# Kernel optimization log

Measured on AMD Instinct MI355X. Metric: run time of the kernel, lower is better.

## Reference

```python
import jax, jax.numpy as jnp
import numpy as np

TOP_K = 2
NUM_EXPERTS = 64
LOAD_BALANCE_ALPHA = 0.01
Z_LOSS_ALPHA = 1e-4
TEMPERATURE = 1.0  # buffer init, clamped to [0.1, 2.0] -> 1.0 (seq_len < 8192 branch)


def setup_inputs() -> dict:
    key = jax.random.key(0)
    k1, k2 = jax.random.split(key)
    x = jax.random.normal(k1, (4, 4096, 1024), dtype=jnp.float32)
    gate_w = jax.random.normal(k2, (NUM_EXPERTS, 1024), dtype=jnp.float32) * (1.0 / np.sqrt(1024))
    return {"x": x, "gate_w": gate_w}


def reference(x, gate_w):
    B, S, H = x.shape
    x_flat = x.reshape(-1, H)                      # [T, H], T = B*S
    logits = jnp.einsum('th,eh->te', x_flat, gate_w)  # [T, E]
    logits = logits / TEMPERATURE
    scores = jax.nn.softmax(logits, axis=-1)       # [T, E]
    # eval path: dynamic_top_k == top_k, no noise / capacity limitation
    top_scores, top_idx = jax.lax.top_k(scores, TOP_K)   # [T, K]
    top_scores = jax.nn.softmax(top_scores.astype(jnp.float32), axis=-1).astype(x.dtype)
    # load-balance loss: squared deviation of mean expert load from uniform
    expert_load = scores.mean(axis=0)              # [E]
    ideal = 1.0 / NUM_EXPERTS
    lb_loss = LOAD_BALANCE_ALPHA * NUM_EXPERTS * jnp.sum((expert_load - ideal) ** 2)
    # z-loss: mean squared logsumexp of gate logits
    z = jax.nn.logsumexp(logits, axis=-1)          # [T]
    z_loss = Z_LOSS_ALPHA * jnp.mean(z ** 2)
    total_loss = lb_loss + z_loss
    return top_scores, top_idx, total_loss
```

## Files before the change

kernel.cpp:

```cpp
#include <hip/hip_runtime.h>
#include <math.h>

#define T_TOK 16384
#define NEXP  64


__global__ void moe_prep(const float* __restrict__ gw, float* __restrict__ ws) {
    __shared__ float tile[64][65];
    const int b = blockIdx.x;
    const int tid = threadIdx.x;
    if (b == 0 && tid < 128) ws[tid] = 0.f;
#pragma unroll
    for (int it = 0; it < 16; ++it) {
        int idx = it * 256 + tid;
        int e = idx >> 6, kk = idx & 63;
        tile[e][kk] = gw[e * 1024 + b * 64 + kk];
    }
    __syncthreads();
#pragma unroll
    for (int it = 0; it < 16; ++it) {
        int idx = it * 256 + tid;
        int kk = idx >> 6, e = idx & 63;
        ws[128 + (b * 64 + kk) * 64 + e] = tile[e][kk];
    }
}

__launch_bounds__(1024, 4)
__global__ void moe_main(const float* __restrict__ x,
                         const float* __restrict__ wt,
                         float* __restrict__ acc_ws,
                         float* __restrict__ out) {
    __shared__ float xbuf[4096];
    __shared__ float wbuf[4096];
    __shared__ float sc[64 * 68];
    __shared__ float row_inv[64];
    __shared__ float colpart[16][64];
    __shared__ int   is_last;

    const int tid  = threadIdx.x;
    const int lane = tid & 63;
    const int wv   = tid >> 6;
    const int kq   = __builtin_amdgcn_readfirstlane(wv & 3);
    const int tile = __builtin_amdgcn_readfirstlane(wv >> 2);
    const int tt = tile >> 1, te = tile & 1;
    const int ta = lane >> 3;
    const int eb = lane & 7;
    const int tok0 = blockIdx.x << 6;

    const int rr = tid >> 4;
    const int cg = tid & 15;
    const float* gx = x + (((size_t)(tok0 + rr)) << 10) + ((cg >> 2) << 8) + ((cg & 3) << 2);
    const int xlo = (rr << 6) + ((cg ^ (rr & 15)) << 2);
    const float* gw = wt + ((((rr >> 4) << 8) + (rr & 15)) << 6) + (cg << 2);
    const int wlo = (rr << 6) + (cg << 2);

    float acc[16];
#pragma unroll
    for (int e = 0; e < 16; ++e) acc[e] = 0.f;

    const int t0 = (tt << 5) + (ta << 2);
    const float* xrow0 = xbuf + ((t0 + 0) << 6);
    const float* xrow1 = xbuf + ((t0 + 1) << 6);
    const float* xrow2 = xbuf + ((t0 + 2) << 6);
    const float* xrow3 = xbuf + ((t0 + 3) << 6);
    const int c0 = (t0 + 0) & 15, c1 = (t0 + 1) & 15;
    const int c2 = (t0 + 2) & 15, c3 = (t0 + 3) & 15;
    const int ebase = (te << 5) + (eb << 2);
    const float* wp = wbuf + (kq << 10) + ebase;
    const int cwb = kq << 2;

    float4 px = *(const float4*)gx;
    float4 pw = *(const float4*)gw;

#pragma unroll 1
    for (int s = 0; s < 16; ++s) {
        __syncthreads();
        *(float4*)(xbuf + xlo) = px;
        *(float4*)(wbuf + wlo) = pw;
        __syncthreads();
        if (s < 15) {
            px = *(const float4*)(gx + ((s + 1) << 4));
            pw = *(const float4*)(gw + ((s + 1) << 10));
        }
#pragma unroll
        for (int g4 = 0; g4 < 4; ++g4) {
            const int cw = cwb + g4;
            float4 xf0 = *(const float4*)(xrow0 + ((cw ^ c0) << 2));
            float4 xf1 = *(const float4*)(xrow1 + ((cw ^ c1) << 2));
            float4 xf2 = *(const float4*)(xrow2 + ((cw ^ c2) << 2));
            float4 xf3 = *(const float4*)(xrow3 + ((cw ^ c3) << 2));
            const float* wq = wp + (g4 << 8);
            float4 wf0 = *(const float4*)(wq);
            float4 wf1 = *(const float4*)(wq + 64);
            float4 wf2 = *(const float4*)(wq + 128);
            float4 wf3 = *(const float4*)(wq + 192);
            float xa[16] = {xf0.x, xf0.y, xf0.z, xf0.w,
                            xf1.x, xf1.y, xf1.z, xf1.w,
                            xf2.x, xf2.y, xf2.z, xf2.w,
                            xf3.x, xf3.y, xf3.z, xf3.w};
            float wa[16] = {wf0.x, wf0.y, wf0.z, wf0.w,
                            wf1.x, wf1.y, wf1.z, wf1.w,
                            wf2.x, wf2.y, wf2.z, wf2.w,
                            wf3.x, wf3.y, wf3.z, wf3.w};
#pragma unroll
            for (int i = 0; i < 4; ++i)
#pragma unroll
                for (int u = 0; u < 4; ++u) {
                    float xv = xa[(i << 2) + u];
#pragma unroll
                    for (int j = 0; j < 4; ++j)
                        acc[(i << 2) + j] = fmaf(xv, wa[(u << 2) + j], acc[(i << 2) + j]);
                }
        }
    }

    if (kq == 0) {
#pragma unroll
        for (int i = 0; i < 4; ++i) {
            float4 v = make_float4(acc[(i << 2)], acc[(i << 2) + 1],
                                   acc[(i << 2) + 2], acc[(i << 2) + 3]);
            *(float4*)(sc + (t0 + i) * 68 + ebase) = v;
        }
    }
    __syncthreads();
    if (kq == 1) {
#pragma unroll
        for (int i = 0; i < 4; ++i) {
            float4 o = *(float4*)(sc + (t0 + i) * 68 + ebase);
            o.x += acc[(i << 2)];     o.y += acc[(i << 2) + 1];
            o.z += acc[(i << 2) + 2]; o.w += acc[(i << 2) + 3];
            *(float4*)(sc + (t0 + i) * 68 + ebase) = o;
        }
    }
    __syncthreads();
    if (kq == 2) {
#pragma unroll
        for (int i = 0; i < 4; ++i) {
            float4 o = *(float4*)(sc + (t0 + i) * 68 + ebase);
            o.x += acc[(i << 2)];     o.y += acc[(i << 2) + 1];
            o.z += acc[(i << 2) + 2]; o.w += acc[(i << 2) + 3];
            *(float4*)(sc + (t0 + i) * 68 + ebase) = o;
        }
    }
    __syncthreads();
    if (kq == 3) {
#pragma unroll
        for (int i = 0; i < 4; ++i) {
            float4 o = *(float4*)(sc + (t0 + i) * 68 + ebase);
            o.x += acc[(i << 2)];     o.y += acc[(i << 2) + 1];
            o.z += acc[(i << 2) + 2]; o.w += acc[(i << 2) + 3];
            *(float4*)(sc + (t0 + i) * 68 + ebase) = o;
        }
    }
    __syncthreads();

    if (tid < 64) {
        const int r = tid;
        const float* srow = sc + r * 68;
        float v1 = -1e30f, v2 = -1e30f;
        int i1 = 0, i2 = 0;
        for (int j = 0; j < 64; ++j) {
            float l = srow[j];
            if (l > v1)      { v2 = v1; i2 = i1; v1 = l; i1 = j; }
            else if (l > v2) { v2 = l; i2 = j; }
        }
        float m = v1;
        float ssum = 0.f;
        for (int j = 0; j < 64; ++j) {
            float ev = expf(srow[j] - m);
            ssum += ev;
            sc[r * 68 + j] = ev;
        }
        float inv = 1.f / ssum;
        row_inv[r] = inv;
        float z = m + logf(ssum);
        float zsq = z * z;
#pragma unroll
        for (int off = 32; off > 0; off >>= 1) zsq += __shfl_down(zsq, off);
        if (lane == 0) atomicAdd(acc_ws + 64, zsq);

        float p1s = inv;
        float p2s = expf(v2 - m) * inv;
        float bb  = expf(p2s - p1s);
        float s1 = 1.f / (1.f + bb);
        float s2 = bb * s1;
        int t = tok0 + r;
        out[2 * t]     = s1;
        out[2 * t + 1] = s2;
        out[2 * T_TOK + 2 * t]     = (float)i1;
        out[2 * T_TOK + 2 * t + 1] = (float)i2;
    }
    __syncthreads();

    {
        int e  = tid & 63;
        int rg = tid >> 6;
        float sum = 0.f;
#pragma unroll
        for (int r2 = 0; r2 < 4; ++r2) {
            int row = (rg << 2) + r2;
            sum += sc[row * 68 + e] * row_inv[row];
        }
        colpart[rg][e] = sum;
    }
    __syncthreads();
    if (tid < 64) {
        float tot = 0.f;
#pragma unroll
        for (int rg = 0; rg < 16; ++rg) tot += colpart[rg][tid];
        atomicAdd(acc_ws + tid, tot);
    }

    __syncthreads();
    if (tid == 0) {
        __threadfence();
        int old = __hip_atomic_fetch_add((int*)(acc_ws + 66), 1,
                                         __ATOMIC_ACQ_REL, __HIP_MEMORY_SCOPE_AGENT);
        is_last = (old == 255) ? 1 : 0;
    }
    __syncthreads();
    if (is_last && tid < 64) {
        __threadfence();
        float load = __hip_atomic_load(acc_ws + tid, __ATOMIC_RELAXED,
                                       __HIP_MEMORY_SCOPE_AGENT) * (1.f / 16384.f);
        float d = load - (1.f / 64.f);
        float v = d * d;
#pragma unroll
        for (int off = 32; off > 0; off >>= 1) v += __shfl_down(v, off);
        if (tid == 0) {
            float zsum = __hip_atomic_load(acc_ws + 64, __ATOMIC_RELAXED,
                                           __HIP_MEMORY_SCOPE_AGENT);
            float lb = 0.01f * 64.f * v;
            float zl = 1e-4f * zsum * (1.f / 16384.f);
            out[4 * T_TOK] = lb + zl;
        }
    }
}

extern "C" void kernel_launch(void* const* d_in, const int* in_sizes, int n_in,
                              void* d_out, int out_size, void* d_ws, size_t ws_size,
                              hipStream_t stream) {
    const float* x  = (const float*)d_in[0];
    const float* gw = (const float*)d_in[1];
    float* out = (float*)d_out;
    float* ws  = (float*)d_ws;

    moe_prep<<<16, 256, 0, stream>>>(gw, ws);
    moe_main<<<256, 1024, 0, stream>>>(x, ws + 128, ws, out);
}
```

Baseline: 133.1 us.

## Split K across all 16 waves with 8x8 register tiles and three-buffer reduction

Each wave now owns a 4-wide K slice of every 64-wide K chunk and computes a full 64x64 token-by-expert tile, with each thread holding an 8x8 accumulator block instead of 4x4. The goal is more FMAs per shared-memory load and simpler LDS addressing: padded rows of 68 floats replace the XOR swizzle, and global loads become contiguous. The cost is that 16 partial tiles must now be summed. This is done in staged rounds into three LDS buffers (sc, xbuf, wbuf) and then merged. The extra barriers, more than 64 accumulator registers under the 1024-thread launch bound, and possible LDS bank conflicts from the strided x reads may offset the gain.

```diff
diff --git a/kernel.cpp b/kernel.cpp
--- a/kernel.cpp
+++ b/kernel.cpp
@@ -25,13 +25,36 @@
     }
 }
 
+__device__ __forceinline__ void pstore(float* B, const float (&a)[8][8],
+                                       int tg, int eg) {
+#pragma unroll
+    for (int i = 0; i < 8; ++i) {
+        float* p = B + (tg + 8 * i) * 68 + (eg << 3);
+        *(float4*)(p)     = make_float4(a[i][0], a[i][1], a[i][2], a[i][3]);
+        *(float4*)(p + 4) = make_float4(a[i][4], a[i][5], a[i][6], a[i][7]);
+    }
+}
+__device__ __forceinline__ void padd(float* B, const float (&a)[8][8],
+                                     int tg, int eg) {
+#pragma unroll
+    for (int i = 0; i < 8; ++i) {
+        float* p = B + (tg + 8 * i) * 68 + (eg << 3);
+        float4 v0 = *(float4*)(p);
+        float4 v1 = *(float4*)(p + 4);
+        v0.x += a[i][0]; v0.y += a[i][1]; v0.z += a[i][2]; v0.w += a[i][3];
+        v1.x += a[i][4]; v1.y += a[i][5]; v1.z += a[i][6]; v1.w += a[i][7];
+        *(float4*)(p)     = v0;
+        *(float4*)(p + 4) = v1;
+    }
+}
+
 __launch_bounds__(1024, 4)
 __global__ void moe_main(const float* __restrict__ x,
                          const float* __restrict__ wt,
                          float* __restrict__ acc_ws,
                          float* __restrict__ out) {
-    __shared__ float xbuf[4096];
-    __shared__ float wbuf[4096];
+    __shared__ float xbuf[64 * 68];
+    __shared__ float wbuf[64 * 68];
     __shared__ float sc[64 * 68];
     __shared__ float row_inv[64];
     __shared__ float colpart[16][64];
@@ -39,35 +62,25 @@
 
     const int tid  = threadIdx.x;
     const int lane = tid & 63;
-    const int wv   = tid >> 6;
-    const int kq   = __builtin_amdgcn_readfirstlane(wv & 3);
-    const int tile = __builtin_amdgcn_readfirstlane(wv >> 2);
-    const int tt = tile >> 1, te = tile & 1;
-    const int ta = lane >> 3;
-    const int eb = lane & 7;
+    const int wv   = __builtin_amdgcn_readfirstlane(tid >> 6);
+    const int tg   = lane & 7;
+    const int eg   = lane >> 3;
     const int tok0 = blockIdx.x << 6;
 
     const int rr = tid >> 4;
     const int cg = tid & 15;
-    const float* gx = x + (((size_t)(tok0 + rr)) << 10) + ((cg >> 2) << 8) + ((cg & 3) << 2);
-    const int xlo = (rr << 6) + ((cg ^ (rr & 15)) << 2);
-    const float* gw = wt + ((((rr >> 4) << 8) + (rr & 15)) << 6) + (cg << 2);
-    const int wlo = (rr << 6) + (cg << 2);
-
-    float acc[16];
-#pragma unroll
-    for (int e = 0; e < 16; ++e) acc[e] = 0.f;
-
-    const int t0 = (tt << 5) + (ta << 2);
-    const float* xrow0 = xbuf + ((t0 + 0) << 6);
-    const float* xrow1 = xbuf + ((t0 + 1) << 6);
-    const float* xrow2 = xbuf + ((t0 + 2) << 6);
-    const float* xrow3 = xbuf + ((t0 + 3) << 6);
-    const int c0 = (t0 + 0) & 15, c1 = (t0 + 1) & 15;
-    const int c2 = (t0 + 2) & 15, c3 = (t0 + 3) & 15;
-    const int ebase = (te << 5) + (eb << 2);
-    const float* wp = wbuf + (kq << 10) + ebase;
-    const int cwb = kq << 2;
+    const float* gx = x + (((size_t)(tok0 + rr)) << 10) + (cg << 2);
+    const float* gw = wt + (rr << 6) + (cg << 2);
+    const int lof = rr * 68 + (cg << 2);
+
+    float acc[8][8];
+#pragma unroll
+    for (int i = 0; i < 8; ++i)
+#pragma unroll
+        for (int j = 0; j < 8; ++j) acc[i][j] = 0.f;
+
+    const float* xr = xbuf + tg * 68 + (wv << 2);
+    const float* wr = wbuf + (wv * 4) * 68 + (eg << 3);
 
     float4 px = *(const float4*)gx;
     float4 pw = *(const float4*)gw;
@@ -75,82 +88,67 @@
 #pragma unroll 1
     for (int s = 0; s < 16; ++s) {
         __syncthreads();
-        *(float4*)(xbuf + xlo) = px;
-        *(float4*)(wbuf + wlo) = pw;
+        *(float4*)(xbuf + lof) = px;
+        *(float4*)(wbuf + lof) = pw;
         __syncthreads();
         if (s < 15) {
-            px = *(const float4*)(gx + ((s + 1) << 4));
-            pw = *(const float4*)(gw + ((s + 1) << 10));
-        }
-#pragma unroll
-        for (int g4 = 0; g4 < 4; ++g4) {
-            const int cw = cwb + g4;
-            float4 xf0 = *(const float4*)(xrow0 + ((cw ^ c0) << 2));
-            float4 xf1 = *(const float4*)(xrow1 + ((cw ^ c1) << 2));
-            float4 xf2 = *(const float4*)(xrow2 + ((cw ^ c2) << 2));
-            float4 xf3 = *(const float4*)(xrow3 + ((cw ^ c3) << 2));
-            const float* wq = wp + (g4 << 8);
-            float4 wf0 = *(const float4*)(wq);
-            float4 wf1 = *(const float4*)(wq + 64);
-            float4 wf2 = *(const float4*)(wq + 128);
-            float4 wf3 = *(const float4*)(wq + 192);
-            float xa[16] = {xf0.x, xf0.y, xf0.z, xf0.w,
-                            xf1.x, xf1.y, xf1.z, xf1.w,
-                            xf2.x, xf2.y, xf2.z, xf2.w,
-                            xf3.x, xf3.y, xf3.z, xf3.w};
-            float wa[16] = {wf0.x, wf0.y, wf0.z, wf0.w,
-                            wf1.x, wf1.y, wf1.z, wf1.w,
-                            wf2.x, wf2.y, wf2.z, wf2.w,
-                            wf3.x, wf3.y, wf3.z, wf3.w};
-#pragma unroll
-            for (int i = 0; i < 4; ++i)
-#pragma unroll
-                for (int u = 0; u < 4; ++u) {
-                    float xv = xa[(i << 2) + u];
-#pragma unroll
-                    for (int j = 0; j < 4; ++j)
-                        acc[(i << 2) + j] = fmaf(xv, wa[(u << 2) + j], acc[(i << 2) + j]);
-                }
-        }
-    }
-
-    if (kq == 0) {
-#pragma unroll
-        for (int i = 0; i < 4; ++i) {
-            float4 v = make_float4(acc[(i << 2)], acc[(i << 2) + 1],
-                                   acc[(i << 2) + 2], acc[(i << 2) + 3]);
-            *(float4*)(sc + (t0 + i) * 68 + ebase) = v;
-        }
-    }
-    __syncthreads();
-    if (kq == 1) {
-#pragma unroll
-        for (int i = 0; i < 4; ++i) {
-            float4 o = *(float4*)(sc + (t0 + i) * 68 + ebase);
-            o.x += acc[(i << 2)];     o.y += acc[(i << 2) + 1];
-            o.z += acc[(i << 2) + 2]; o.w += acc[(i << 2) + 3];
-            *(float4*)(sc + (t0 + i) * 68 + ebase) = o;
-        }
-    }
-    __syncthreads();
-    if (kq == 2) {
-#pragma unroll
-        for (int i = 0; i < 4; ++i) {
-            float4 o = *(float4*)(sc + (t0 + i) * 68 + ebase);
-            o.x += acc[(i << 2)];     o.y += acc[(i << 2) + 1];
-            o.z += acc[(i << 2) + 2]; o.w += acc[(i << 2) + 3];
-            *(float4*)(sc + (t0 + i) * 68 + ebase) = o;
-        }
-    }
-    __syncthreads();
-    if (kq == 3) {
-#pragma unroll
-        for (int i = 0; i < 4; ++i) {
-            float4 o = *(float4*)(sc + (t0 + i) * 68 + ebase);
-            o.x += acc[(i << 2)];     o.y += acc[(i << 2) + 1];
-            o.z += acc[(i << 2) + 2]; o.w += acc[(i << 2) + 3];
-            *(float4*)(sc + (t0 + i) * 68 + ebase) = o;
-        }
+            px = *(const float4*)(gx + ((s + 1) << 6));
+            pw = *(const float4*)(gw + ((s + 1) << 12));
+        }
+        float wa[4][8];
+#pragma unroll
+        for (int u = 0; u < 4; ++u) {
+            float4 q0 = *(const float4*)(wr + u * 68);
+            float4 q1 = *(const float4*)(wr + u * 68 + 4);
+            wa[u][0] = q0.x; wa[u][1] = q0.y; wa[u][2] = q0.z; wa[u][3] = q0.w;
+            wa[u][4] = q1.x; wa[u][5] = q1.y; wa[u][6] = q1.z; wa[u][7] = q1.w;
+        }
+#pragma unroll
+        for (int i = 0; i < 8; ++i) {
+            float4 xc = *(const float4*)(xr + i * 544);
+            float xa[4] = {xc.x, xc.y, xc.z, xc.w};
+#pragma unroll
+            for (int u = 0; u < 4; ++u) {
+                float xv = xa[u];
+#pragma unroll
+                for (int j = 0; j < 8; ++j)
+                    acc[i][j] = fmaf(xv, wa[u][j], acc[i][j]);
+            }
+        }
+    }
+
+    __syncthreads();
+    if      (wv == 0) pstore(sc,   acc, tg, eg);
+    else if (wv == 1) pstore(xbuf, acc, tg, eg);
+    else if (wv == 2) pstore(wbuf, acc, tg, eg);
+    __syncthreads();
+    if      (wv == 3) padd(sc,   acc, tg, eg);
+    else if (wv == 4) padd(xbuf, acc, tg, eg);
+    else if (wv == 5) padd(wbuf, acc, tg, eg);
+    __syncthreads();
+    if      (wv == 6) padd(sc,   acc, tg, eg);
+    else if (wv == 7) padd(xbuf, acc, tg, eg);
+    else if (wv == 8) padd(wbuf, acc, tg, eg);
+    __syncthreads();
+    if      (wv == 9)  padd(sc,   acc, tg, eg);
+    else if (wv == 10) padd(xbuf, acc, tg, eg);
+    else if (wv == 11) padd(wbuf, acc, tg, eg);
+    __syncthreads();
+    if      (wv == 12) padd(sc,   acc, tg, eg);
+    else if (wv == 13) padd(xbuf, acc, tg, eg);
+    else if (wv == 14) padd(wbuf, acc, tg, eg);
+    __syncthreads();
+    if (wv == 15) padd(sc, acc, tg, eg);
+    __syncthreads();
+    {
+        const int row = tid >> 4, g = tid & 15;
+        float* ps = sc + row * 68 + (g << 2);
+        float4 a  = *(float4*)ps;
+        float4 bx = *(const float4*)(xbuf + row * 68 + (g << 2));
+        float4 bw = *(const float4*)(wbuf + row * 68 + (g << 2));
+        a.x += bx.x + bw.x; a.y += bx.y + bw.y;
+        a.z += bx.z + bw.z; a.w += bx.w + bw.w;
+        *(float4*)ps = a;
     }
     __syncthreads();
 
```

After: 131.0 us. No clear change (-1.6%).

## Read gate weights as wave-uniform scalar loads and stage only x in LDS

Applied to the files above, without the earlier changes.

Restructures the GEMM inner loop so each lane owns one token and 16 experts. Weight rows are read directly from global memory at wave-uniform addresses, which lets them go through scalar loads and the constant cache instead of LDS. x is staged in a padded 64x260 LDS tile in 4 larger stages rather than 16, which halves the barrier count per stage and drops the weight LDS buffer. In exchange, each x float4 read from LDS now feeds only 16 FMAs. The scalar weight loads also sit on the critical path, and launch bounds drop to 1 block per CU.

```diff
diff --git a/kernel.cpp b/kernel.cpp
--- a/kernel.cpp
+++ b/kernel.cpp
@@ -25,13 +25,12 @@
     }
 }
 
-__launch_bounds__(1024, 4)
+__launch_bounds__(1024, 1)
 __global__ void moe_main(const float* __restrict__ x,
                          const float* __restrict__ wt,
                          float* __restrict__ acc_ws,
                          float* __restrict__ out) {
-    __shared__ float xbuf[4096];
-    __shared__ float wbuf[4096];
+    __shared__ float xbuf[64 * 260];
     __shared__ float sc[64 * 68];
     __shared__ float row_inv[64];
     __shared__ float colpart[16][64];
@@ -41,118 +40,95 @@
     const int lane = tid & 63;
     const int wv   = tid >> 6;
     const int kq   = __builtin_amdgcn_readfirstlane(wv & 3);
-    const int tile = __builtin_amdgcn_readfirstlane(wv >> 2);
-    const int tt = tile >> 1, te = tile & 1;
-    const int ta = lane >> 3;
-    const int eb = lane & 7;
+    const int eg   = __builtin_amdgcn_readfirstlane(wv >> 2);
     const int tok0 = blockIdx.x << 6;
 
     const int rr = tid >> 4;
     const int cg = tid & 15;
-    const float* gx = x + (((size_t)(tok0 + rr)) << 10) + ((cg >> 2) << 8) + ((cg & 3) << 2);
-    const int xlo = (rr << 6) + ((cg ^ (rr & 15)) << 2);
-    const float* gw = wt + ((((rr >> 4) << 8) + (rr & 15)) << 6) + (cg << 2);
-    const int wlo = (rr << 6) + (cg << 2);
+    const float* gx = x + (((size_t)(tok0 + rr)) << 10) + (cg << 2);
+    float* xw = xbuf + rr * 260 + (cg << 2);
 
     float acc[16];
 #pragma unroll
-    for (int e = 0; e < 16; ++e) acc[e] = 0.f;
-
-    const int t0 = (tt << 5) + (ta << 2);
-    const float* xrow0 = xbuf + ((t0 + 0) << 6);
-    const float* xrow1 = xbuf + ((t0 + 1) << 6);
-    const float* xrow2 = xbuf + ((t0 + 2) << 6);
-    const float* xrow3 = xbuf + ((t0 + 3) << 6);
-    const int c0 = (t0 + 0) & 15, c1 = (t0 + 1) & 15;
-    const int c2 = (t0 + 2) & 15, c3 = (t0 + 3) & 15;
-    const int ebase = (te << 5) + (eb << 2);
-    const float* wp = wbuf + (kq << 10) + ebase;
-    const int cwb = kq << 2;
-
-    float4 px = *(const float4*)gx;
-    float4 pw = *(const float4*)gw;
+    for (int j = 0; j < 16; ++j) acc[j] = 0.f;
+
+    const float* xb = xbuf + lane * 260 + (kq << 6);
+
+    float4 px0 = *(const float4*)(gx);
+    float4 px1 = *(const float4*)(gx + 64);
+    float4 px2 = *(const float4*)(gx + 128);
+    float4 px3 = *(const float4*)(gx + 192);
 
 #pragma unroll 1
-    for (int s = 0; s < 16; ++s) {
+    for (int s = 0; s < 4; ++s) {
         __syncthreads();
-        *(float4*)(xbuf + xlo) = px;
-        *(float4*)(wbuf + wlo) = pw;
+        *(float4*)(xw)       = px0;
+        *(float4*)(xw + 64)  = px1;
+        *(float4*)(xw + 128) = px2;
+        *(float4*)(xw + 192) = px3;
         __syncthreads();
-        if (s < 15) {
-            px = *(const float4*)(gx + ((s + 1) << 4));
-            pw = *(const float4*)(gw + ((s + 1) << 10));
-        }
-#pragma unroll
-        for (int g4 = 0; g4 < 4; ++g4) {
-            const int cw = cwb + g4;
-            float4 xf0 = *(const float4*)(xrow0 + ((cw ^ c0) << 2));
-            float4 xf1 = *(const float4*)(xrow1 + ((cw ^ c1) << 2));
-            float4 xf2 = *(const float4*)(xrow2 + ((cw ^ c2) << 2));
-            float4 xf3 = *(const float4*)(xrow3 + ((cw ^ c3) << 2));
-            const float* wq = wp + (g4 << 8);
-            float4 wf0 = *(const float4*)(wq);
-            float4 wf1 = *(const float4*)(wq + 64);
-            float4 wf2 = *(const float4*)(wq + 128);
-            float4 wf3 = *(const float4*)(wq + 192);
-            float xa[16] = {xf0.x, xf0.y, xf0.z, xf0.w,
-                            xf1.x, xf1.y, xf1.z, xf1.w,
-                            xf2.x, xf2.y, xf2.z, xf2.w,
-                            xf3.x, xf3.y, xf3.z, xf3.w};
-            float wa[16] = {wf0.x, wf0.y, wf0.z, wf0.w,
-                            wf1.x, wf1.y, wf1.z, wf1.w,
-                            wf2.x, wf2.y, wf2.z, wf2.w,
-                            wf3.x, wf3.y, wf3.z, wf3.w};
-#pragma unroll
-            for (int i = 0; i < 4; ++i)
-#pragma unroll
-                for (int u = 0; u < 4; ++u) {
-                    float xv = xa[(i << 2) + u];
-#pragma unroll
-                    for (int j = 0; j < 4; ++j)
-                        acc[(i << 2) + j] = fmaf(xv, wa[(u << 2) + j], acc[(i << 2) + j]);
-                }
-        }
-    }
-
+        if (s < 3) {
+            const int o = (s + 1) << 8;
+            px0 = *(const float4*)(gx + o);
+            px1 = *(const float4*)(gx + o + 64);
+            px2 = *(const float4*)(gx + o + 128);
+            px3 = *(const float4*)(gx + o + 192);
+        }
+        const int krow0 = __builtin_amdgcn_readfirstlane((s << 8) + (kq << 6));
+        const float* wslab = wt + (krow0 << 6) + (eg << 4);
+#pragma unroll
+        for (int c = 0; c < 16; ++c) {
+            float4 xv = *(const float4*)(xb + (c << 2));
+            float xa[4] = {xv.x, xv.y, xv.z, xv.w};
+#pragma unroll
+            for (int u = 0; u < 4; ++u) {
+                const float* wr = wslab + (((c << 2) + u) << 6);
+                float4 w0 = *(const float4*)(wr);
+                float4 w1 = *(const float4*)(wr + 4);
+                float4 w2 = *(const float4*)(wr + 8);
+                float4 w3 = *(const float4*)(wr + 12);
+                const float xs = xa[u];
+                acc[0]  = fmaf(xs, w0.x, acc[0]);
+                acc[1]  = fmaf(xs, w0.y, acc[1]);
+                acc[2]  = fmaf(xs, w0.z, acc[2]);
+                acc[3]  = fmaf(xs, w0.w, acc[3]);
+                acc[4]  = fmaf(xs, w1.x, acc[4]);
+                acc[5]  = fmaf(xs, w1.y, acc[5]);
+                acc[6]  = fmaf(xs, w1.z, acc[6]);
+                acc[7]  = fmaf(xs, w1.w, acc[7]);
+                acc[8]  = fmaf(xs, w2.x, acc[8]);
+                acc[9]  = fmaf(xs, w2.y, acc[9]);
+                acc[10] = fmaf(xs, w2.z, acc[10]);
+                acc[11] = fmaf(xs, w2.w, acc[11]);
+                acc[12] = fmaf(xs, w3.x, acc[12]);
+                acc[13] = fmaf(xs, w3.y, acc[13]);
+                acc[14] = fmaf(xs, w3.z, acc[14]);
+                acc[15] = fmaf(xs, w3.w, acc[15]);
+            }
+        }
+    }
+
+    float* sp = sc + lane * 68 + (eg << 4);
     if (kq == 0) {
-#pragma unroll
-        for (int i = 0; i < 4; ++i) {
-            float4 v = make_float4(acc[(i << 2)], acc[(i << 2) + 1],
-                                   acc[(i << 2) + 2], acc[(i << 2) + 3]);
-            *(float4*)(sc + (t0 + i) * 68 + ebase) = v;
-        }
-    }
-    __syncthreads();
-    if (kq == 1) {
-#pragma unroll
-        for (int i = 0; i < 4; ++i) {
-            float4 o = *(float4*)(sc + (t0 + i) * 68 + ebase);
-            o.x += acc[(i << 2)];     o.y += acc[(i << 2) + 1];
-            o.z += acc[(i << 2) + 2]; o.w += acc[(i << 2) + 3];
-            *(float4*)(sc + (t0 + i) * 68 + ebase) = o;
-        }
-    }
-    __syncthreads();
-    if (kq == 2) {
-#pragma unroll
-        for (int i = 0; i < 4; ++i) {
-            float4 o = *(float4*)(sc + (t0 + i) * 68 + ebase);
-            o.x += acc[(i << 2)];     o.y += acc[(i << 2) + 1];
-            o.z += acc[(i << 2) + 2]; o.w += acc[(i << 2) + 3];
-            *(float4*)(sc + (t0 + i) * 68 + ebase) = o;
-        }
-    }
-    __syncthreads();
-    if (kq == 3) {
-#pragma unroll
-        for (int i = 0; i < 4; ++i) {
-            float4 o = *(float4*)(sc + (t0 + i) * 68 + ebase);
-            o.x += acc[(i << 2)];     o.y += acc[(i << 2) + 1];
-            o.z += acc[(i << 2) + 2]; o.w += acc[(i << 2) + 3];
-            *(float4*)(sc + (t0 + i) * 68 + ebase) = o;
-        }
-    }
-    __syncthreads();
+        *(float4*)(sp)      = make_float4(acc[0], acc[1], acc[2], acc[3]);
+        *(float4*)(sp + 4)  = make_float4(acc[4], acc[5], acc[6], acc[7]);
+        *(float4*)(sp + 8)  = make_float4(acc[8], acc[9], acc[10], acc[11]);
+        *(float4*)(sp + 12) = make_float4(acc[12], acc[13], acc[14], acc[15]);
+    }
+    __syncthreads();
+#pragma unroll 1
+    for (int r = 1; r < 4; ++r) {
+        if (kq == r) {
+#pragma unroll
+            for (int g = 0; g < 4; ++g) {
+                float4 o = *(float4*)(sp + (g << 2));
+                o.x += acc[(g << 2)];     o.y += acc[(g << 2) + 1];
+                o.z += acc[(g << 2) + 2]; o.w += acc[(g << 2) + 3];
+                *(float4*)(sp + (g << 2)) = o;
+            }
+        }
+        __syncthreads();
+    }
 
     if (tid < 64) {
         const int r = tid;
```

After: 134.0 us. About the same (+0.7%).
